# Performance work log

Measured on AMD Instinct MI355X. Metric: run time of the kernel, lower is better.

Reference implementation:

```python
import jax, jax.numpy as jnp
import numpy as np

DIM = 1024
HEADS = 16
DHEAD = 64
INNER = HEADS * DHEAD
B, N = 1, 2048
ROPE_BASE = 10000.0
LN_EPS = 1e-5


def rope_tables(seq_len, d, dtype):
    # theta_i = 1 / base^(2i/d); emb = cat(freqs, freqs) -> cos/sin [N, d]
    theta = 1.0 / (ROPE_BASE ** (jnp.arange(0, d, 2, dtype=dtype) / d))
    pos = jnp.arange(seq_len, dtype=dtype)
    freqs = pos[:, None] * theta[None, :]          # [N, d/2]
    emb = jnp.concatenate([freqs, freqs], axis=-1)  # [N, d]
    return jnp.cos(emb), jnp.sin(emb)


def apply_rotary(x, cos, sin):
    # x: [B,H,N,D], cos/sin: [N,D]; interleaved rotation as in the torch code
    x1, x2 = x[..., ::2], x[..., 1::2]
    x_rot = jnp.stack([-x2, x1], axis=-1).reshape(x.shape)
    return x * cos + x_rot * sin


def setup_inputs() -> dict:
    key = jax.random.key(0)
    ks = jax.random.split(key, 6)
    x = jax.random.normal(ks[0], (B, N, DIM), dtype=jnp.float32)
    gamma = jnp.ones((DIM,), dtype=jnp.float32)
    Wq = jax.random.normal(ks[1], (DIM, INNER), dtype=jnp.float32) * 0.02
    Wkv = jax.random.normal(ks[2], (DIM, 2 * INNER), dtype=jnp.float32) * 0.02
    # near-identity per-head bilinear transform (torch inits toward identity)
    W_bilinear = jnp.eye(DHEAD, dtype=jnp.float32)[None] + \
        jax.random.normal(ks[3], (HEADS, DHEAD, DHEAD), dtype=jnp.float32) * 0.02
    Wo = jax.random.normal(ks[4], (INNER, DIM), dtype=jnp.float32) * 0.02
    return {"x": x, "gamma": gamma, "Wq": Wq, "Wkv": Wkv,
            "W_bilinear": W_bilinear, "Wo": Wo}


def reference(x, gamma, Wq, Wkv, W_bilinear, Wo):
    b, n, _ = x.shape
    # LayerNorm (beta = 0 buffer)
    mu = jnp.mean(x, axis=-1, keepdims=True)
    var = jnp.var(x, axis=-1, keepdims=True)
    xn = (x - mu) / jnp.sqrt(var + LN_EPS) * gamma

    q = xn @ Wq                                    # [B,N,INNER]
    kv = xn @ Wkv                                  # [B,N,2*INNER]
    k, v = jnp.split(kv, 2, axis=-1)

    def to_heads(t):
        return t.reshape(b, n, HEADS, DHEAD).transpose(0, 2, 1, 3)  # [B,H,N,D]

    q, k, v = map(to_heads, (q, k, v))

    cos, sin = rope_tables(n, DHEAD, x.dtype)
    q = apply_rotary(q, cos, sin) * (DHEAD ** -0.5)
    k = apply_rotary(k, cos, sin)

    # per-head bilinear transform of K
    kt = jnp.einsum('bhnd,hde->bhne', k, W_bilinear)
    sim = jnp.einsum('bhid,bhjd->bhij', q, kt)      # [B,H,N,N]
    attn = jax.nn.softmax(sim, axis=-1)
    out = jnp.einsum('bhij,bhjd->bhid', attn, v)    # [B,H,N,D]
    out = out.transpose(0, 2, 1, 3).reshape(b, n, INNER)
    return out @ Wo
```

## Files before the change

kernel.cpp:

```cpp
#include <hip/hip_runtime.h>
#include <hip/hip_bf16.h>


typedef unsigned short u16;
typedef __attribute__((ext_vector_type(4))) float f32x4;
typedef __attribute__((ext_vector_type(8))) __bf16 bf16x8;

struct alignas(8) US4 { u16 x, y, z, w; };

__device__ __forceinline__ u16 f2bf(float f) {
  union { float f; unsigned u; } v; v.f = f;
  unsigned r = v.u + 0x7FFFu + ((v.u >> 16) & 1u);
  return (u16)(r >> 16);
}
__device__ __forceinline__ unsigned pk2bf(float a, float b) {
  float2 f; f.x = a; f.y = b;
  __hip_bfloat162 h = __float22bfloat162_rn(f);
  union { __hip_bfloat162 h; unsigned u; } v; v.h = h;
  return v.u;
}

typedef void GVOID __attribute__((address_space(1)));
typedef void LVOID __attribute__((address_space(3)));

#if defined(__has_builtin)
#if __has_builtin(__builtin_amdgcn_global_load_lds)
#define HAS_GLD_LDS 1
#endif
#endif

__device__ __forceinline__ void gld16(const void* g, void* l) {
#ifdef HAS_GLD_LDS
  __builtin_amdgcn_global_load_lds((GVOID*)(void*)g, (LVOID*)l, 16, 0, 0);
#else
  struct alignas(16) U4 { unsigned a, b, c, d; };
  *(U4*)l = *(const U4*)g;
#endif
}

__device__ __forceinline__ f32x4 MFMA(bf16x8 a, bf16x8 b, f32x4 c) {
  return __builtin_amdgcn_mfma_f32_16x16x32_bf16(a, b, c, 0, 0, 0);
}

__device__ __forceinline__ int swz(int r, int q) {
  return r * 32 + ((q ^ ((r >> 1) & 3)) << 3);
}
__device__ __forceinline__ int swz_src_colb(int o) {
  const int r = o >> 6;
  return ((((o >> 4) & 3) ^ ((r >> 1) & 3)) << 4);
}
__device__ __forceinline__ int mswz4(int ee, int c) {
  return ee * 64 + ((c ^ (ee & 15)) << 2);
}
__device__ __forceinline__ int mswz1(int ee, int q) {
  return ee * 64 + ((((q >> 2) ^ (ee & 15)) << 2) | (q & 3));
}

__global__ __launch_bounds__(256) void prep_kernel(
    const float* __restrict__ x, const float* __restrict__ gamma,
    const float* __restrict__ Wq, const float* __restrict__ Wkv,
    const float* __restrict__ Wo, const float* __restrict__ Wb,
    u16* __restrict__ xn, u16* __restrict__ wqkvT, u16* __restrict__ woT,
    u16* __restrict__ wbT) {
  __shared__ __align__(16) float smem[64 * 65];
  const int bid = blockIdx.x, t = threadIdx.x;
  if (bid < 1040) {
    const float* src; u16* dst; int C, R, bx, by;
    if (bid < 256)      { src = Wq;  dst = wqkvT; R = 1024; C = 1024; bx = bid & 15; by = bid >> 4; }
    else if (bid < 768) { int i = bid - 256; src = Wkv; dst = wqkvT + 1024 * 1024; R = 1024; C = 2048; bx = i & 31; by = i >> 5; }
    else if (bid < 1024){ int i = bid - 768; src = Wo;  dst = woT; R = 1024; C = 1024; bx = i & 15; by = i >> 4; }
    else { int h = bid - 1024; src = Wb + (size_t)h * 4096; dst = wbT + (size_t)h * 4096; R = 64; C = 64; bx = 0; by = 0; }
    float (*tile)[65] = (float(*)[65])smem;
    const int c0 = bx * 64, r0 = by * 64;
    const int tx = t & 63, ty = t >> 6;
#pragma unroll
    for (int i = 0; i < 16; i++)
      tile[ty + i * 4][tx] = src[(size_t)(r0 + ty + i * 4) * C + c0 + tx];
    __syncthreads();
#pragma unroll
    for (int i = 0; i < 16; i++)
      dst[(size_t)(c0 + ty + i * 4) * R + r0 + tx] = f2bf(tile[tx][ty + i * 4]);
  } else {
    const int n = bid - 1040;
    const int w = t >> 6, lane = t & 63;
    const float4 v = *(const float4*)&x[(size_t)n * 1024 + t * 4];
    float s = v.x + v.y + v.z + v.w;
    float q = v.x * v.x + v.y * v.y + v.z * v.z + v.w * v.w;
#pragma unroll
    for (int off = 32; off; off >>= 1) {
      s += __shfl_down(s, off);
      q += __shfl_down(q, off);
    }
    if (lane == 0) { smem[w] = s; smem[4 + w] = q; }
    __syncthreads();
    s = smem[0] + smem[1] + smem[2] + smem[3];
    q = smem[4] + smem[5] + smem[6] + smem[7];
    const float mean = s * (1.0f / 1024.0f);
    const float var = q * (1.0f / 1024.0f) - mean * mean;
    const float inv = rsqrtf(var + 1e-5f);
    const float4 g = *(const float4*)&gamma[t * 4];
    US4 o;
    o.x = f2bf((v.x - mean) * inv * g.x);
    o.y = f2bf((v.y - mean) * inv * g.y);
    o.z = f2bf((v.z - mean) * inv * g.z);
    o.w = f2bf((v.w - mean) * inv * g.w);
    *(US4*)&xn[(size_t)n * 1024 + t * 4] = o;
  }
}

__global__ __launch_bounds__(256, 2) void gemm_qkv(
    const u16* __restrict__ A, const u16* __restrict__ B,
    const u16* __restrict__ wbT, u16* __restrict__ qh,
    u16* __restrict__ kth, u16* __restrict__ vt) {
  __shared__ u16 As[2 * 64 * 32];
  __shared__ u16 Bs[2 * 128 * 32];
  __shared__ u16 krs[2 * 4096];
  const int K = 1024;
  const int t = threadIdx.x;
  const int w = t >> 6, lane = t & 63, quad = lane >> 4, cc = lane & 15;
  const int bm = blockIdx.y << 6, bn = blockIdx.x << 7;
  const int wm = (w >> 1) << 5, wn = (w & 1) << 6;
  const f32x4 fzero = {0.f, 0.f, 0.f, 0.f};
  f32x4 acc[2][4];
#pragma unroll
  for (int i = 0; i < 2; i++)
#pragma unroll
    for (int j = 0; j < 4; j++) acc[i][j] = fzero;

  const char* gA = (const char*)A;
  const char* gB = (const char*)B;
  for (int k0 = 0; k0 < K; k0 += 64) {
    __syncthreads();
#pragma unroll
    for (int i = 0; i < 2; i++) {
      const int o = (i * 256 + t) * 16;
      const int sub = o >> 12, row = (o >> 6) & 63, colb = swz_src_colb(o);
      gld16(gA + (((size_t)(bm + row) * K + k0 + sub * 32) << 1) + colb, (char*)As + o);
    }
#pragma unroll
    for (int i = 0; i < 4; i++) {
      const int o = (i * 256 + t) * 16;
      const int sub = o >> 13, row = (o >> 6) & 127, colb = swz_src_colb(o);
      gld16(gB + (((size_t)(bn + row) * K + k0 + sub * 32) << 1) + colb, (char*)Bs + o);
    }
    __syncthreads();
#pragma unroll
    for (int ks = 0; ks < 2; ks++) {
      bf16x8 af[2], bfr[4];
#pragma unroll
      for (int mi = 0; mi < 2; mi++)
        af[mi] = *(const bf16x8*)&As[ks * 2048 + swz(wm + mi * 16 + cc, quad)];
#pragma unroll
      for (int ni = 0; ni < 4; ni++)
        bfr[ni] = *(const bf16x8*)&Bs[ks * 4096 + swz(wn + ni * 16 + cc, quad)];
#pragma unroll
      for (int mi = 0; mi < 2; mi++)
#pragma unroll
        for (int ni = 0; ni < 4; ni++)
          acc[mi][ni] = MFMA(af[mi], bfr[ni], acc[mi][ni]);
    }
  }

  const int region = blockIdx.x >> 3;
  if (region == 0) {
#pragma unroll
    for (int ni = 0; ni < 4; ni++) {
      const int col = bn + wn + ni * 16 + cc;
      const int h = (col >> 6) & 15, d = col & 63;
      const float theta = __expf(-(float)(col & 31) * 0.2878231366242557f);
      const float sgn = (col & 1) ? 1.0f : -1.0f;
#pragma unroll
      for (int mi = 0; mi < 2; mi++) {
        const int row0 = bm + wm + mi * 16 + quad * 4;
#pragma unroll
        for (int r = 0; r < 4; r++) {
          const float val = acc[mi][ni][r];
          const float pr = __shfl_xor(val, 1);
          float sv, cv;
          __sincosf(theta * (float)(row0 + r), &sv, &cv);
          qh[((size_t)h * 2048 + row0 + r) * 64 + d] =
              f2bf((val * cv + sgn * pr * sv) * 0.125f);
        }
      }
    }
  } else if (region == 2) {
#pragma unroll
    for (int ni = 0; ni < 4; ni++) {
      const int col = bn + wn + ni * 16 + cc;
      const int h = (col >> 6) & 15, d = col & 63;
      u16* base = vt + ((size_t)h * 64 + d) * 2048;
#pragma unroll
      for (int mi = 0; mi < 2; mi++) {
        const int row0 = bm + wm + mi * 16 + quad * 4;
        uint2 pk;
        pk.x = pk2bf(acc[mi][ni][0], acc[mi][ni][1]);
        pk.y = pk2bf(acc[mi][ni][2], acc[mi][ni][3]);
        *(uint2*)&base[row0] = pk;
      }
    }
  } else {
    const int h2 = w & 1;
    u16* krh = krs + h2 * 4096;
#pragma unroll
    for (int ni = 0; ni < 4; ni++) {
      const int dloc = ni * 16 + cc;
      const int dsub = dloc >> 5;
      const int chunk = (dloc & 31) >> 3, elem = dloc & 7;
      const int col = bn + wn + ni * 16 + cc;
      const float theta = __expf(-(float)(col & 31) * 0.2878231366242557f);
      const float sgn = (col & 1) ? 1.0f : -1.0f;
#pragma unroll
      for (int mi = 0; mi < 2; mi++) {
        const int lrow0 = wm + mi * 16 + quad * 4;
#pragma unroll
        for (int r = 0; r < 4; r++) {
          const float val = acc[mi][ni][r];
          const float pr = __shfl_xor(val, 1);
          float sv, cv;
          __sincosf(theta * (float)(bm + lrow0 + r), &sv, &cv);
          const int row = lrow0 + r;
          krh[dsub * 2048 + row * 32 + ((chunk ^ ((row >> 1) & 3)) << 3) + elem] =
              f2bf(val * cv + sgn * pr * sv);
        }
      }
    }
    __syncthreads();
    const int hg0 = (bn >> 6) & 15;
#pragma unroll
    for (int i = 0; i < 2; i++) {
      const int o = (i * 256 + t) * 16;
      const int row = o >> 6;
      const int dsub = row >> 6, e = row & 63;
      const int colb = swz_src_colb(o);
      gld16((const char*)wbT + (((size_t)hg0 * 4096 + e * 64 + dsub * 32) << 1) + colb,
            (char*)As + o);
      gld16((const char*)wbT + (((size_t)(hg0 + 1) * 4096 + e * 64 + dsub * 32) << 1) + colb,
            (char*)Bs + o);
    }
    __syncthreads();
    const int wmrow = (w >> 1) << 5;
    const u16* Bsel = h2 ? Bs : As;
    f32x4 acc2[2][4];
#pragma unroll
    for (int i = 0; i < 2; i++)
#pragma unroll
      for (int j = 0; j < 4; j++) acc2[i][j] = fzero;
#pragma unroll
    for (int dsub = 0; dsub < 2; dsub++) {
      bf16x8 bfr[4];
#pragma unroll
      for (int et = 0; et < 4; et++)
        bfr[et] = *(const bf16x8*)&Bsel[swz(dsub * 64 + et * 16 + cc, quad)];
#pragma unroll
      for (int mi = 0; mi < 2; mi++) {
        const bf16x8 af = *(const bf16x8*)&krh[dsub * 2048 + swz(wmrow + mi * 16 + cc, quad)];
#pragma unroll
        for (int et = 0; et < 4; et++)
          acc2[mi][et] = MFMA(af, bfr[et], acc2[mi][et]);
      }
    }
    u16* Ck = kth + (size_t)(hg0 + h2) * 2048 * 64;
#pragma unroll
    for (int mi = 0; mi < 2; mi++) {
      const int n0 = bm + wmrow + mi * 16 + quad * 4;
#pragma unroll
      for (int et = 0; et < 4; et++) {
        const int e = et * 16 + cc;
#pragma unroll
        for (int r = 0; r < 4; r++)
          Ck[(size_t)(n0 + r) * 64 + e] = f2bf(acc2[mi][et][r]);
      }
    }
  }
}

__global__ __launch_bounds__(256, 2) void attn_kernel(
    const u16* __restrict__ qh, const u16* __restrict__ kth,
    const u16* __restrict__ vt, u16* __restrict__ aout) {
  __shared__ __align__(16) u16 lds[40960];
  u16* const Kb0 = lds;
  u16* const Kb1 = lds + 8192;
  u16* const Vb0 = lds + 16384;
  u16* const Vb1 = lds + 24576;
  u16* const Ps  = lds + 32768;
  const int t = threadIdx.x;
  const int w = t >> 6, lane = t & 63, quad = lane >> 4, cc = lane & 15;
  const int bid = blockIdx.x;
  const int h = (bid & 7) + ((bid >> 8) << 3);
  const int q0 = ((bid >> 3) & 31) << 6;
  const size_t hq = (size_t)h * (2048 * 64);
  const f32x4 fzero = {0.f, 0.f, 0.f, 0.f};
  const int g4 = (cc >> 1) & 3;

  bf16x8 ones;
  {
    union { u16 u; __bf16 b; } one; one.u = 0x3F80;
#pragma unroll
    for (int i = 0; i < 8; i++) ones[i] = one.b;
  }

  bf16x8 qf[4][2];
  f32x4 oacc[4][4];
  f32x4 lacc[4];
#pragma unroll
  for (int mi = 0; mi < 4; mi++) {
    lacc[mi] = fzero;
#pragma unroll
    for (int et = 0; et < 4; et++) oacc[mi][et] = fzero;
  }

  u16* const psw = Ps + (w << 11);

  auto PREFETCH = [&](int jtn, u16* KD, u16* VD) {
    const int j0n = jtn << 7;
#pragma unroll
    for (int i = 0; i < 4; i++) {
      const int o = (i * 256 + t) * 16;
      const int colb = swz_src_colb(o);
      const int sub = o >> 13, row = (o >> 6) & 127;
      gld16((const char*)kth + ((hq + (size_t)(j0n + row) * 64 + sub * 32) << 1) + colb,
            (char*)KD + o);
      const int vsub = o >> 12, vrow = (o >> 6) & 63;
      gld16((const char*)vt + ((hq + (size_t)vrow * 2048 + j0n + vsub * 32) << 1) + colb,
            (char*)VD + o);
    }
  };

  auto COMPUTE = [&](const u16* KS, const u16* VS) {
#pragma unroll
    for (int jm = 0; jm < 2; jm++) {
      const bf16x8 kf0 = *(const bf16x8*)&KS[swz(w * 32 + jm * 16 + cc, quad)];
      const bf16x8 kf1 = *(const bf16x8*)&KS[swz(128 + w * 32 + jm * 16 + cc, quad)];
      const int c16 = ((jm << 1) + (quad >> 1)) ^ g4;
      const int coff = (c16 << 3) + ((quad & 1) << 2);
#pragma unroll
      for (int qn = 0; qn < 4; qn++) {
        f32x4 s = MFMA(kf0, qf[qn][0], fzero);
        s = MFMA(kf1, qf[qn][1], s);
        uint2 pk;
        pk.x = pk2bf(__expf(s[0]), __expf(s[1]));
        pk.y = pk2bf(__expf(s[2]), __expf(s[3]));
        *(uint2*)&psw[((qn * 16 + cc) << 5) + coff] = pk;
      }
    }
    bf16x8 vf[4];
#pragma unroll
    for (int et = 0; et < 4; et++)
      vf[et] = *(const bf16x8*)&VS[swz(w * 64 + et * 16 + cc, quad)];
#pragma unroll
    for (int mi = 0; mi < 4; mi++) {
      const bf16x8 pa = *(const bf16x8*)&psw[swz(mi * 16 + cc, quad)];
      lacc[mi] = MFMA(pa, ones, lacc[mi]);
#pragma unroll
      for (int et = 0; et < 4; et++) oacc[mi][et] = MFMA(pa, vf[et], oacc[mi][et]);
    }
  };

#pragma unroll
  for (int i = 0; i < 2; i++) {
    const int o = (i * 256 + t) * 16;
    const int sub = o >> 12, row = (o >> 6) & 63, colb = swz_src_colb(o);
    gld16((const char*)qh + ((hq + (size_t)(q0 + row) * 64 + sub * 32) << 1) + colb,
          (char*)Ps + o);
  }
  PREFETCH(0, Kb0, Vb0);
  __syncthreads();
#pragma unroll
  for (int qn = 0; qn < 4; qn++)
#pragma unroll
    for (int ds = 0; ds < 2; ds++)
      qf[qn][ds] = *(const bf16x8*)&Ps[swz(ds * 64 + qn * 16 + cc, quad)];
  __syncthreads();

  for (int jt = 0; jt < 16; jt += 2) {
    PREFETCH(jt + 1, Kb1, Vb1);
    COMPUTE(Kb0, Vb0);
    __syncthreads();
    if (jt + 2 < 16) PREFETCH(jt + 2, Kb0, Vb0);
    COMPUTE(Kb1, Vb1);
    __syncthreads();
  }

  float* OA = (float*)Kb0;
  float* OB = (float*)Kb1;
  float* lP = (float*)Vb0;
  if (w >= 2) {
    float* dst = (w == 2) ? OA : OB;
#pragma unroll
    for (int mi = 0; mi < 4; mi++) {
#pragma unroll
      for (int et = 0; et < 4; et++) {
        const int ee = et * 16 + cc;
        *(f32x4*)&dst[mswz4(ee, mi * 4 + quad)] = oacc[mi][et];
      }
      if (cc == 0)
#pragma unroll
        for (int r = 0; r < 4; r++)
          lP[64 * w + mi * 16 + quad * 4 + r] = lacc[mi][r];
    }
  }
  __syncthreads();
  if (w < 2) {
    const float* src = (w == 0) ? OA : OB;
    const float* lsrc = &lP[64 * (w + 2)];
#pragma unroll
    for (int mi = 0; mi < 4; mi++) {
#pragma unroll
      for (int et = 0; et < 4; et++) {
        const int ee = et * 16 + cc;
        oacc[mi][et] += *(const f32x4*)&src[mswz4(ee, mi * 4 + quad)];
      }
#pragma unroll
      for (int r = 0; r < 4; r++)
        lacc[mi][r] += lsrc[mi * 16 + quad * 4 + r];
    }
  }
  __syncthreads();
  if (w < 2) {
    float* dst = (w == 0) ? OA : OB;
#pragma unroll
    for (int mi = 0; mi < 4; mi++) {
#pragma unroll
      for (int et = 0; et < 4; et++) {
        const int ee = et * 16 + cc;
        *(f32x4*)&dst[mswz4(ee, mi * 4 + quad)] = oacc[mi][et];
      }
      if (cc == 0)
#pragma unroll
        for (int r = 0; r < 4; r++)
          lP[64 * w + mi * 16 + quad * 4 + r] = lacc[mi][r];
    }
  }
  __syncthreads();
  {
    const int q = lane;
    const float linv = 1.0f / (lP[q] + lP[64 + q]);
    unsigned obuf[8];
#pragma unroll
    for (int e = 0; e < 8; e++) {
      const int e0 = w * 16 + e * 2, e1 = e0 + 1;
      obuf[e] = pk2bf((OA[mswz1(e0, q)] + OB[mswz1(e0, q)]) * linv,
                      (OA[mswz1(e1, q)] + OB[mswz1(e1, q)]) * linv);
    }
    uint4* dst = (uint4*)&aout[(size_t)(q0 + q) * 1024 + h * 64 + w * 16];
    dst[0] = *(uint4*)&obuf[0];
    dst[1] = *(uint4*)&obuf[4];
  }
}

__global__ __launch_bounds__(256, 2) void gemm64_bt_f32(
    const u16* __restrict__ A, const u16* __restrict__ B, float* __restrict__ C,
    int M, int N, int K) {
  __shared__ u16 As[4 * 64 * 32];
  __shared__ u16 Bs[4 * 64 * 32];
  const int t = threadIdx.x;
  const int w = t >> 6, lane = t & 63, quad = lane >> 4, cc = lane & 15;
  const int bm = blockIdx.y << 6, bn = blockIdx.x << 6;
  const int wm = (w >> 1) << 5, wn = (w & 1) << 5;
  const f32x4 fzero = {0.f, 0.f, 0.f, 0.f};
  f32x4 acc[2][2];
#pragma unroll
  for (int i = 0; i < 2; i++)
#pragma unroll
    for (int j = 0; j < 2; j++) acc[i][j] = fzero;

  const char* gA = (const char*)A;
  const char* gB = (const char*)B;
  for (int k0 = 0; k0 < K; k0 += 128) {
    __syncthreads();
#pragma unroll
    for (int i = 0; i < 4; i++) {
      const int o = (i * 256 + t) * 16;
      const int sub = o >> 12, row = (o >> 6) & 63, colb = swz_src_colb(o);
      gld16(gA + (((size_t)(bm + row) * K + k0 + sub * 32) << 1) + colb, (char*)As + o);
      gld16(gB + (((size_t)(bn + row) * K + k0 + sub * 32) << 1) + colb, (char*)Bs + o);
    }
    __syncthreads();
#pragma unroll
    for (int ks = 0; ks < 4; ks++) {
      bf16x8 af[2], bfr[2];
#pragma unroll
      for (int mi = 0; mi < 2; mi++)
        af[mi] = *(const bf16x8*)&As[ks * 2048 + swz(wm + mi * 16 + cc, quad)];
#pragma unroll
      for (int ni = 0; ni < 2; ni++)
        bfr[ni] = *(const bf16x8*)&Bs[ks * 2048 + swz(wn + ni * 16 + cc, quad)];
#pragma unroll
      for (int mi = 0; mi < 2; mi++)
#pragma unroll
        for (int ni = 0; ni < 2; ni++)
          acc[mi][ni] = MFMA(af[mi], bfr[ni], acc[mi][ni]);
    }
  }
#pragma unroll
  for (int mi = 0; mi < 2; mi++) {
    const int row = bm + wm + mi * 16 + quad * 4;
#pragma unroll
    for (int ni = 0; ni < 2; ni++) {
      const int col = bn + wn + ni * 16 + cc;
#pragma unroll
      for (int r = 0; r < 4; r++) C[(size_t)(row + r) * N + col] = acc[mi][ni][r];
    }
  }
}

extern "C" void kernel_launch(void* const* d_in, const int* in_sizes, int n_in,
                              void* d_out, int out_size, void* d_ws, size_t ws_size,
                              hipStream_t stream) {
  (void)in_sizes; (void)n_in; (void)out_size; (void)ws_size;
  const float* x     = (const float*)d_in[0];
  const float* gamma = (const float*)d_in[1];
  const float* Wq    = (const float*)d_in[2];
  const float* Wkv   = (const float*)d_in[3];
  const float* Wb    = (const float*)d_in[4];
  const float* Wo    = (const float*)d_in[5];
  float* out = (float*)d_out;
  char* ws = (char*)d_ws;

  const size_t OFF_XN    = 0;
  const size_t OFF_WQKVT = 4194304;
  const size_t OFF_WOT   = 10485760;
  const size_t OFF_WBT   = 12582912;
  const size_t OFF_QH    = 12713984;
  const size_t OFF_KTH   = 16908288;
  const size_t OFF_VT    = 21102592;
  const size_t OFF_AOUT  = 25296896;

  u16* xn    = (u16*)(ws + OFF_XN);
  u16* wqkvT = (u16*)(ws + OFF_WQKVT);
  u16* woT   = (u16*)(ws + OFF_WOT);
  u16* wbT   = (u16*)(ws + OFF_WBT);
  u16* qh    = (u16*)(ws + OFF_QH);
  u16* kth   = (u16*)(ws + OFF_KTH);
  u16* vt    = (u16*)(ws + OFF_VT);
  u16* aout  = (u16*)(ws + OFF_AOUT);

  prep_kernel<<<3088, 256, 0, stream>>>(x, gamma, Wq, Wkv, Wo, Wb,
                                        xn, wqkvT, woT, wbT);
  gemm_qkv<<<dim3(24, 32), 256, 0, stream>>>(xn, wqkvT, wbT, qh, kth, vt);
  attn_kernel<<<512, 256, 0, stream>>>(qh, kth, vt, aout);
  gemm64_bt_f32<<<dim3(16, 32), 256, 0, stream>>>(aout, woT, out, 2048, 1024, 1024);
}
```

Before: 140.0 us.

## Halve attention query tile to 32 rows and drop double buffering for occupancy

The attention kernel now handles 32 query rows per block instead of 64, doubling the grid to 1024 blocks. It replaces the double-buffered K/V staging with a single buffer, which halves LDS use, and raises the launch bound to 4 blocks per CU. The aim is more resident waves to hide latency, and better CU fill on a large-CU GPU. In exchange, each block reloads K/V for half as many queries, so global/L2 traffic doubles, and loads no longer overlap with compute within a block.

New measurement: 145.0 us. 3.5% more time.

```diff
diff --git a/kernel.cpp b/kernel.cpp
--- a/kernel.cpp
+++ b/kernel.cpp
@@ -54,6 +54,12 @@
 }
 __device__ __forceinline__ int mswz1(int ee, int q) {
   return ee * 64 + ((((q >> 2) ^ (ee & 15)) << 2) | (q & 3));
+}
+__device__ __forceinline__ int m32_4(int ee, int c) {
+  return ee * 32 + ((c ^ (ee & 7)) << 2);
+}
+__device__ __forceinline__ int m32_1(int ee, int q) {
+  return ee * 32 + ((((q >> 2) ^ (ee & 7)) << 2) | (q & 3));
 }
 
 __global__ __launch_bounds__(256) void prep_kernel(
@@ -274,20 +280,18 @@
   }
 }
 
-__global__ __launch_bounds__(256, 2) void attn_kernel(
+__global__ __launch_bounds__(256, 4) void attn_kernel(
     const u16* __restrict__ qh, const u16* __restrict__ kth,
     const u16* __restrict__ vt, u16* __restrict__ aout) {
-  __shared__ __align__(16) u16 lds[40960];
-  u16* const Kb0 = lds;
-  u16* const Kb1 = lds + 8192;
-  u16* const Vb0 = lds + 16384;
-  u16* const Vb1 = lds + 24576;
-  u16* const Ps  = lds + 32768;
+  __shared__ __align__(16) u16 lds[20480];
+  u16* const Ks = lds;
+  u16* const Vs = lds + 8192;
+  u16* const Ps = lds + 16384;
   const int t = threadIdx.x;
   const int w = t >> 6, lane = t & 63, quad = lane >> 4, cc = lane & 15;
   const int bid = blockIdx.x;
-  const int h = (bid & 7) + ((bid >> 8) << 3);
-  const int q0 = ((bid >> 3) & 31) << 6;
+  const int h = (bid & 7) + ((bid >> 9) << 3);
+  const int q0 = ((bid >> 3) & 63) << 5;
   const size_t hq = (size_t)h * (2048 * 64);
   const f32x4 fzero = {0.f, 0.f, 0.f, 0.f};
   const int g4 = (cc >> 1) & 3;
@@ -299,42 +303,56 @@
     for (int i = 0; i < 8; i++) ones[i] = one.b;
   }
 
-  bf16x8 qf[4][2];
-  f32x4 oacc[4][4];
-  f32x4 lacc[4];
-#pragma unroll
-  for (int mi = 0; mi < 4; mi++) {
+  bf16x8 qf[2][2];
+  f32x4 oacc[2][4];
+  f32x4 lacc[2];
+#pragma unroll
+  for (int mi = 0; mi < 2; mi++) {
     lacc[mi] = fzero;
 #pragma unroll
     for (int et = 0; et < 4; et++) oacc[mi][et] = fzero;
   }
 
-  u16* const psw = Ps + (w << 11);
-
-  auto PREFETCH = [&](int jtn, u16* KD, u16* VD) {
-    const int j0n = jtn << 7;
+  u16* const psw = Ps + (w << 10);
+
+  {
+    const int o = t * 16;
+    const int sub = o >> 11, row = (o >> 6) & 31, colb = swz_src_colb(o);
+    gld16((const char*)qh + ((hq + (size_t)(q0 + row) * 64 + sub * 32) << 1) + colb,
+          (char*)Ps + o);
+  }
+  __syncthreads();
+#pragma unroll
+  for (int qn = 0; qn < 2; qn++)
+#pragma unroll
+    for (int ds = 0; ds < 2; ds++)
+      qf[qn][ds] = *(const bf16x8*)&Ps[swz(ds * 32 + qn * 16 + cc, quad)];
+  __syncthreads();
+
+  for (int jt = 0; jt < 16; jt++) {
+    const int j0 = jt << 7;
+    __syncthreads();
 #pragma unroll
     for (int i = 0; i < 4; i++) {
       const int o = (i * 256 + t) * 16;
       const int colb = swz_src_colb(o);
       const int sub = o >> 13, row = (o >> 6) & 127;
-      gld16((const char*)kth + ((hq + (size_t)(j0n + row) * 64 + sub * 32) << 1) + colb,
-            (char*)KD + o);
+      gld16((const char*)kth + ((hq + (size_t)(j0 + row) * 64 + sub * 32) << 1) + colb,
+            (char*)Ks + o);
       const int vsub = o >> 12, vrow = (o >> 6) & 63;
-      gld16((const char*)vt + ((hq + (size_t)vrow * 2048 + j0n + vsub * 32) << 1) + colb,
-            (char*)VD + o);
-    }
-  };
-
-  auto COMPUTE = [&](const u16* KS, const u16* VS) {
+      gld16((const char*)vt + ((hq + (size_t)vrow * 2048 + j0 + vsub * 32) << 1) + colb,
+            (char*)Vs + o);
+    }
+    __syncthreads();
+
 #pragma unroll
     for (int jm = 0; jm < 2; jm++) {
-      const bf16x8 kf0 = *(const bf16x8*)&KS[swz(w * 32 + jm * 16 + cc, quad)];
-      const bf16x8 kf1 = *(const bf16x8*)&KS[swz(128 + w * 32 + jm * 16 + cc, quad)];
+      const bf16x8 kf0 = *(const bf16x8*)&Ks[swz(w * 32 + jm * 16 + cc, quad)];
+      const bf16x8 kf1 = *(const bf16x8*)&Ks[swz(128 + w * 32 + jm * 16 + cc, quad)];
       const int c16 = ((jm << 1) + (quad >> 1)) ^ g4;
       const int coff = (c16 << 3) + ((quad & 1) << 2);
 #pragma unroll
-      for (int qn = 0; qn < 4; qn++) {
+      for (int qn = 0; qn < 2; qn++) {
         f32x4 s = MFMA(kf0, qf[qn][0], fzero);
         s = MFMA(kf1, qf[qn][1], s);
         uint2 pk;
@@ -343,72 +361,49 @@
         *(uint2*)&psw[((qn * 16 + cc) << 5) + coff] = pk;
       }
     }
+
     bf16x8 vf[4];
 #pragma unroll
     for (int et = 0; et < 4; et++)
-      vf[et] = *(const bf16x8*)&VS[swz(w * 64 + et * 16 + cc, quad)];
-#pragma unroll
-    for (int mi = 0; mi < 4; mi++) {
+      vf[et] = *(const bf16x8*)&Vs[swz(w * 64 + et * 16 + cc, quad)];
+#pragma unroll
+    for (int mi = 0; mi < 2; mi++) {
       const bf16x8 pa = *(const bf16x8*)&psw[swz(mi * 16 + cc, quad)];
       lacc[mi] = MFMA(pa, ones, lacc[mi]);
 #pragma unroll
       for (int et = 0; et < 4; et++) oacc[mi][et] = MFMA(pa, vf[et], oacc[mi][et]);
     }
-  };
-
-#pragma unroll
-  for (int i = 0; i < 2; i++) {
-    const int o = (i * 256 + t) * 16;
-    const int sub = o >> 12, row = (o >> 6) & 63, colb = swz_src_colb(o);
-    gld16((const char*)qh + ((hq + (size_t)(q0 + row) * 64 + sub * 32) << 1) + colb,
-          (char*)Ps + o);
-  }
-  PREFETCH(0, Kb0, Vb0);
+  }
+
+  float* OA = (float*)Ks;
+  float* OB = (float*)Vs;
+  float* lP = (float*)Ps;
   __syncthreads();
-#pragma unroll
-  for (int qn = 0; qn < 4; qn++)
-#pragma unroll
-    for (int ds = 0; ds < 2; ds++)
-      qf[qn][ds] = *(const bf16x8*)&Ps[swz(ds * 64 + qn * 16 + cc, quad)];
-  __syncthreads();
-
-  for (int jt = 0; jt < 16; jt += 2) {
-    PREFETCH(jt + 1, Kb1, Vb1);
-    COMPUTE(Kb0, Vb0);
-    __syncthreads();
-    if (jt + 2 < 16) PREFETCH(jt + 2, Kb0, Vb0);
-    COMPUTE(Kb1, Vb1);
-    __syncthreads();
-  }
-
-  float* OA = (float*)Kb0;
-  float* OB = (float*)Kb1;
-  float* lP = (float*)Vb0;
   if (w >= 2) {
     float* dst = (w == 2) ? OA : OB;
 #pragma unroll
-    for (int mi = 0; mi < 4; mi++) {
+    for (int mi = 0; mi < 2; mi++) {
 #pragma unroll
       for (int et = 0; et < 4; et++) {
         const int ee = et * 16 + cc;
-        *(f32x4*)&dst[mswz4(ee, mi * 4 + quad)] = oacc[mi][et];
+        *(f32x4*)&dst[m32_4(ee, mi * 4 + quad)] = oacc[mi][et];
       }
       if (cc == 0)
 #pragma unroll
         for (int r = 0; r < 4; r++)
-          lP[64 * w + mi * 16 + quad * 4 + r] = lacc[mi][r];
+          lP[32 * w + mi * 16 + quad * 4 + r] = lacc[mi][r];
     }
   }
   __syncthreads();
   if (w < 2) {
     const float* src = (w == 0) ? OA : OB;
-    const float* lsrc = &lP[64 * (w + 2)];
-#pragma unroll
-    for (int mi = 0; mi < 4; mi++) {
+    const float* lsrc = &lP[32 * (w + 2)];
+#pragma unroll
+    for (int mi = 0; mi < 2; mi++) {
 #pragma unroll
       for (int et = 0; et < 4; et++) {
         const int ee = et * 16 + cc;
-        oacc[mi][et] += *(const f32x4*)&src[mswz4(ee, mi * 4 + quad)];
+        oacc[mi][et] += *(const f32x4*)&src[m32_4(ee, mi * 4 + quad)];
       }
 #pragma unroll
       for (int r = 0; r < 4; r++)
@@ -419,32 +414,31 @@
   if (w < 2) {
     float* dst = (w == 0) ? OA : OB;
 #pragma unroll
-    for (int mi = 0; mi < 4; mi++) {
+    for (int mi = 0; mi < 2; mi++) {
 #pragma unroll
       for (int et = 0; et < 4; et++) {
         const int ee = et * 16 + cc;
-        *(f32x4*)&dst[mswz4(ee, mi * 4 + quad)] = oacc[mi][et];
+        *(f32x4*)&dst[m32_4(ee, mi * 4 + quad)] = oacc[mi][et];
       }
       if (cc == 0)
 #pragma unroll
         for (int r = 0; r < 4; r++)
-          lP[64 * w + mi * 16 + quad * 4 + r] = lacc[mi][r];
+          lP[32 * w + mi * 16 + quad * 4 + r] = lacc[mi][r];
     }
   }
   __syncthreads();
   {
-    const int q = lane;
-    const float linv = 1.0f / (lP[q] + lP[64 + q]);
-    unsigned obuf[8];
-#pragma unroll
-    for (int e = 0; e < 8; e++) {
-      const int e0 = w * 16 + e * 2, e1 = e0 + 1;
-      obuf[e] = pk2bf((OA[mswz1(e0, q)] + OB[mswz1(e0, q)]) * linv,
-                      (OA[mswz1(e1, q)] + OB[mswz1(e1, q)]) * linv);
-    }
-    uint4* dst = (uint4*)&aout[(size_t)(q0 + q) * 1024 + h * 64 + w * 16];
-    dst[0] = *(uint4*)&obuf[0];
-    dst[1] = *(uint4*)&obuf[4];
+    const int q = lane & 31, eh = lane >> 5;
+    const float linv = 1.0f / (lP[q] + lP[32 + q]);
+    unsigned obuf[4];
+#pragma unroll
+    for (int e = 0; e < 4; e++) {
+      const int e0 = w * 16 + eh * 8 + e * 2, e1 = e0 + 1;
+      obuf[e] = pk2bf((OA[m32_1(e0, q)] + OB[m32_1(e0, q)]) * linv,
+                      (OA[m32_1(e1, q)] + OB[m32_1(e1, q)]) * linv);
+    }
+    *(uint4*)&aout[(size_t)(q0 + q) * 1024 + h * 64 + w * 16 + eh * 8] =
+        *(uint4*)&obuf[0];
   }
 }
 
@@ -538,6 +532,6 @@
   prep_kernel<<<3088, 256, 0, stream>>>(x, gamma, Wq, Wkv, Wo, Wb,
                                         xn, wqkvT, woT, wbT);
   gemm_qkv<<<dim3(24, 32), 256, 0, stream>>>(xn, wqkvT, wbT, qh, kth, vt);
-  attn_kernel<<<512, 256, 0, stream>>>(qh, kth, vt, aout);
+  attn_kernel<<<1024, 256, 0, stream>>>(qh, kth, vt, aout);
   gemm64_bt_f32<<<dim3(16, 32), 256, 0, stream>>>(aout, woT, out, 2048, 1024, 1024);
 }
```

## Single-buffer K/V tiles in attention to raise occupancy to three blocks per CU

Applied to the files above, without the earlier changes.

Replaces the double-buffered K/V LDS pipeline with a single buffer, loading each tile and synchronizing before computing on it. Q fragments are now read straight from global memory instead of being staged through LDS. LDS drops from 80KB to 48KB per block and launch bounds go from 2 to 3 blocks per CU, so other resident blocks are meant to hide load latency. In exchange, the explicit overlap of prefetch with compute is lost and the register budget per thread is tighter.

New measurement: 141.9 us. About the same (+1.4%).

```diff
diff --git a/kernel.cpp b/kernel.cpp
--- a/kernel.cpp
+++ b/kernel.cpp
@@ -274,15 +274,13 @@
   }
 }
 
-__global__ __launch_bounds__(256, 2) void attn_kernel(
+__global__ __launch_bounds__(256, 3) void attn_kernel(
     const u16* __restrict__ qh, const u16* __restrict__ kth,
     const u16* __restrict__ vt, u16* __restrict__ aout) {
-  __shared__ __align__(16) u16 lds[40960];
-  u16* const Kb0 = lds;
-  u16* const Kb1 = lds + 8192;
-  u16* const Vb0 = lds + 16384;
-  u16* const Vb1 = lds + 24576;
-  u16* const Ps  = lds + 32768;
+  __shared__ __align__(16) u16 lds[24576];
+  u16* const Ks = lds;
+  u16* const Vs = lds + 8192;
+  u16* const Ps = lds + 16384;
   const int t = threadIdx.x;
   const int w = t >> 6, lane = t & 63, quad = lane >> 4, cc = lane & 15;
   const int bid = blockIdx.x;
@@ -300,6 +298,13 @@
   }
 
   bf16x8 qf[4][2];
+#pragma unroll
+  for (int qn = 0; qn < 4; qn++)
+#pragma unroll
+    for (int ds = 0; ds < 2; ds++)
+      qf[qn][ds] = *(const bf16x8*)&qh[hq + (size_t)(q0 + qn * 16 + cc) * 64 +
+                                       ds * 32 + quad * 8];
+
   f32x4 oacc[4][4];
   f32x4 lacc[4];
 #pragma unroll
@@ -311,26 +316,26 @@
 
   u16* const psw = Ps + (w << 11);
 
-  auto PREFETCH = [&](int jtn, u16* KD, u16* VD) {
-    const int j0n = jtn << 7;
+  for (int jt = 0; jt < 16; jt++) {
+    const int j0 = jt << 7;
+    __syncthreads();
 #pragma unroll
     for (int i = 0; i < 4; i++) {
       const int o = (i * 256 + t) * 16;
       const int colb = swz_src_colb(o);
       const int sub = o >> 13, row = (o >> 6) & 127;
-      gld16((const char*)kth + ((hq + (size_t)(j0n + row) * 64 + sub * 32) << 1) + colb,
-            (char*)KD + o);
+      gld16((const char*)kth + ((hq + (size_t)(j0 + row) * 64 + sub * 32) << 1) + colb,
+            (char*)Ks + o);
       const int vsub = o >> 12, vrow = (o >> 6) & 63;
-      gld16((const char*)vt + ((hq + (size_t)vrow * 2048 + j0n + vsub * 32) << 1) + colb,
-            (char*)VD + o);
-    }
-  };
-
-  auto COMPUTE = [&](const u16* KS, const u16* VS) {
+      gld16((const char*)vt + ((hq + (size_t)vrow * 2048 + j0 + vsub * 32) << 1) + colb,
+            (char*)Vs + o);
+    }
+    __syncthreads();
+
 #pragma unroll
     for (int jm = 0; jm < 2; jm++) {
-      const bf16x8 kf0 = *(const bf16x8*)&KS[swz(w * 32 + jm * 16 + cc, quad)];
-      const bf16x8 kf1 = *(const bf16x8*)&KS[swz(128 + w * 32 + jm * 16 + cc, quad)];
+      const bf16x8 kf0 = *(const bf16x8*)&Ks[swz(w * 32 + jm * 16 + cc, quad)];
+      const bf16x8 kf1 = *(const bf16x8*)&Ks[swz(128 + w * 32 + jm * 16 + cc, quad)];
       const int c16 = ((jm << 1) + (quad >> 1)) ^ g4;
       const int coff = (c16 << 3) + ((quad & 1) << 2);
 #pragma unroll
@@ -343,10 +348,11 @@
         *(uint2*)&psw[((qn * 16 + cc) << 5) + coff] = pk;
       }
     }
+
     bf16x8 vf[4];
 #pragma unroll
     for (int et = 0; et < 4; et++)
-      vf[et] = *(const bf16x8*)&VS[swz(w * 64 + et * 16 + cc, quad)];
+      vf[et] = *(const bf16x8*)&Vs[swz(w * 64 + et * 16 + cc, quad)];
 #pragma unroll
     for (int mi = 0; mi < 4; mi++) {
       const bf16x8 pa = *(const bf16x8*)&psw[swz(mi * 16 + cc, quad)];
@@ -354,36 +360,12 @@
 #pragma unroll
       for (int et = 0; et < 4; et++) oacc[mi][et] = MFMA(pa, vf[et], oacc[mi][et]);
     }
-  };
-
-#pragma unroll
-  for (int i = 0; i < 2; i++) {
-    const int o = (i * 256 + t) * 16;
-    const int sub = o >> 12, row = (o >> 6) & 63, colb = swz_src_colb(o);
-    gld16((const char*)qh + ((hq + (size_t)(q0 + row) * 64 + sub * 32) << 1) + colb,
-          (char*)Ps + o);
-  }
-  PREFETCH(0, Kb0, Vb0);
+  }
+
+  float* OA = (float*)Ks;
+  float* OB = (float*)Vs;
+  float* lP = (float*)Ps;
   __syncthreads();
-#pragma unroll
-  for (int qn = 0; qn < 4; qn++)
-#pragma unroll
-    for (int ds = 0; ds < 2; ds++)
-      qf[qn][ds] = *(const bf16x8*)&Ps[swz(ds * 64 + qn * 16 + cc, quad)];
-  __syncthreads();
-
-  for (int jt = 0; jt < 16; jt += 2) {
-    PREFETCH(jt + 1, Kb1, Vb1);
-    COMPUTE(Kb0, Vb0);
-    __syncthreads();
-    if (jt + 2 < 16) PREFETCH(jt + 2, Kb0, Vb0);
-    COMPUTE(Kb1, Vb1);
-    __syncthreads();
-  }
-
-  float* OA = (float*)Kb0;
-  float* OB = (float*)Kb1;
-  float* lP = (float*)Vb0;
   if (w >= 2) {
     float* dst = (w == 2) ? OA : OB;
 #pragma unroll
```
